# Kernel tuning notes

Measured on AMD Instinct MI355X. Metric: run time of the kernel, lower is better.

The kernel has to match this reference:

```python
import jax, jax.numpy as jnp
import numpy as np

D_IN = 1024
D_OUT = 1024
NUM_HEADS = 16
HEAD_DIM = D_OUT // NUM_HEADS


def setup_inputs() -> dict:
    key = jax.random.key(0)
    ks = jax.random.split(key, 6)
    s = 0.02
    x = jax.random.normal(ks[0], (2, 2048, D_IN), dtype=jnp.float32)
    wq = jax.random.normal(ks[1], (D_IN, D_OUT), dtype=jnp.float32) * s
    wk = jax.random.normal(ks[2], (D_IN, D_OUT), dtype=jnp.float32) * s
    wv = jax.random.normal(ks[3], (D_IN, D_OUT), dtype=jnp.float32) * s
    wo = jax.random.normal(ks[4], (D_OUT, D_OUT), dtype=jnp.float32) * s
    bo = jax.random.normal(ks[5], (D_OUT,), dtype=jnp.float32) * s
    return {"x": x, "wq": wq, "wk": wk, "wv": wv, "wo": wo, "bo": bo}


def reference(x, wq, wk, wv, wo, bo):
    B, S, _ = x.shape
    # QKV projections (no bias, qkv_bias=False)
    def split_heads(t):
        return t.reshape(B, S, NUM_HEADS, HEAD_DIM).transpose(0, 2, 1, 3)  # [B,H,S,Dh]
    q = split_heads(x @ wq)
    k = split_heads(x @ wk)
    v = split_heads(x @ wv)
    scores = jnp.einsum('bhqd,bhkd->bhqk', q, k) / np.sqrt(HEAD_DIM).astype(np.float32)
    causal = jnp.tril(jnp.ones((S, S), dtype=bool))  # [S,S]
    scores = jnp.where(causal[None, None], scores, -jnp.inf)
    attn = jax.nn.softmax(scores, axis=-1)  # dropout p=0.0 -> identity
    ctx = jnp.einsum('bhqk,bhkd->bhqd', attn, v)
    ctx = ctx.transpose(0, 2, 1, 3).reshape(B, S, D_OUT)
    return ctx @ wo + bo
```

## Files before the change

kernel.cpp:

```cpp
#include <hip/hip_runtime.h>

typedef short s16x8 __attribute__((ext_vector_type(8)));
typedef float f32x4 __attribute__((ext_vector_type(4)));
typedef float f32x16 __attribute__((ext_vector_type(16)));
typedef unsigned int u32;
typedef u32 u32x2 __attribute__((ext_vector_type(2)));
typedef u32 u32x4 __attribute__((ext_vector_type(4)));
typedef unsigned short u16;

#define MFMA16(a, b, c) __builtin_amdgcn_mfma_f32_16x16x32_bf16((a), (b), (c), 0, 0, 0)
#define MFMA32(a, b, c) __builtin_amdgcn_mfma_f32_32x32x16_bf16((a), (b), (c), 0, 0, 0)

__device__ __forceinline__ u16 f2bf(float f) {
  unsigned u = __builtin_bit_cast(unsigned, f);
  unsigned r = (u + 0x7FFFu + ((u >> 16) & 1u)) >> 16;
  return (u16)r;
}

__device__ __forceinline__ u32 pack2bf(float lo, float hi) {
  return (u32)f2bf(lo) | ((u32)f2bf(hi) << 16);
}

__device__ __forceinline__ u32 cvtpk(float lo, float hi) {
  u32 r;
  asm("v_cvt_pk_bf16_f32 %0, %1, %2" : "=v"(r) : "v"(lo), "v"(hi));
  return r;
}

__device__ __forceinline__ float bf2f(u32 lo16) {
  return __builtin_bit_cast(float, lo16 << 16);
}

__device__ __forceinline__ void gl_lds16(const u16* g, u16* s) {
  __builtin_amdgcn_global_load_lds(
      (const __attribute__((address_space(1))) void*)g,
      (__attribute__((address_space(3))) void*)s, 16, 0, 0);
}

__global__ __launch_bounds__(256) void cvt_bf16(const float* __restrict__ in,
                                                u16* __restrict__ out, int n4) {
  int i = blockIdx.x * 256 + threadIdx.x;
  if (i < n4) {
    float4 v = reinterpret_cast<const float4*>(in)[i];
    ushort4 o;
    o.x = f2bf(v.x); o.y = f2bf(v.y); o.z = f2bf(v.z); o.w = f2bf(v.w);
    reinterpret_cast<ushort4*>(out)[i] = o;
  }
}

__global__ __launch_bounds__(256) void transp4(const float* __restrict__ wq,
                                               const float* __restrict__ wk,
                                               const float* __restrict__ wv,
                                               const float* __restrict__ wo,
                                               u16* __restrict__ wqkvt,
                                               u16* __restrict__ wot, float qscale) {
  __shared__ float tile[64][65];
  int z = blockIdx.z;
  const float* W = (z == 0) ? wq : (z == 1) ? wk : (z == 2) ? wv : wo;
  u16* out = (z < 3) ? (wqkvt + z * 1048576) : wot;
  float sc = (z == 0) ? qscale : 1.0f;
  int n0 = blockIdx.x * 64, k0 = blockIdx.y * 64;
  int t = threadIdx.x;
#pragma unroll
  for (int i = 0; i < 16; i++) {
    int idx = t + i * 256;
    int r = idx >> 6, c = idx & 63;
    tile[r][c] = W[(k0 + r) * 1024 + (n0 + c)];
  }
  __syncthreads();
#pragma unroll
  for (int i = 0; i < 16; i++) {
    int idx = t + i * 256;
    int r = idx >> 6, c = idx & 63;
    out[(n0 + r) * 1024 + (k0 + c)] = f2bf(tile[c][r] * sc);
  }
}

template <int MODE>
__global__ __launch_bounds__(256, 6) void gemm2(const u16* __restrict__ A,
                                                const u16* __restrict__ Bt,
                                                const float* __restrict__ bias,
                                                void* __restrict__ outp) {
  constexpr int K = 1024, NT = K / 32;
  __shared__ __align__(16) u16 shm[12288];
  int t = threadIdx.x, w = t >> 6, l = t & 63;
  int m0 = blockIdx.y * 64, n0 = blockIdx.x * 128;
  int wm = (w >> 1) * 32, wn = (w & 1) * 64;
  int g = l >> 4, ql = l & 15;
  int xs = (g ^ ((ql >> 1) & 3)) * 8;

  f32x4 acc[2][4];
#pragma unroll
  for (int i = 0; i < 2; i++)
#pragma unroll
    for (int j = 0; j < 4; j++) acc[i][j] = f32x4{0.f, 0.f, 0.f, 0.f};

  int lrow = l >> 2, lcol = ((l & 3) ^ ((l >> 3) & 3)) * 8;
  const u16* Ag0 = A + (m0 + 16 * w + lrow) * K + lcol;
  const u16* Bg0 = Bt + (n0 + 32 * w + lrow) * K + lcol;
  u16* Asw[2] = {shm + 16 * w * 32, shm + 2048 + 16 * w * 32};
  u16* Bsw[2] = {shm + 4096 + 32 * w * 32, shm + 8192 + 32 * w * 32};

#define STAGE(buf, kt)                              \
  do {                                              \
    int k0_ = (kt) * 32;                            \
    gl_lds16(Ag0 + k0_, Asw[buf]);                  \
    gl_lds16(Bg0 + k0_, Bsw[buf]);                  \
    gl_lds16(Bg0 + 16 * K + k0_, Bsw[buf] + 512);   \
  } while (0)

#define COMPUTE(buf)                                                              \
  do {                                                                            \
    const u16* As_ = shm + (buf)*2048;                                            \
    const u16* Bs_ = shm + 4096 + (buf)*4096;                                     \
    s16x8 af[2], bv[4];                                                           \
    _Pragma("unroll") for (int fm = 0; fm < 2; fm++)                              \
        af[fm] = *reinterpret_cast<const s16x8*>(                                 \
            &As_[(wm + fm * 16 + ql) * 32 + xs]);                                 \
    _Pragma("unroll") for (int fn = 0; fn < 4; fn++)                              \
        bv[fn] = *reinterpret_cast<const s16x8*>(                                 \
            &Bs_[(wn + fn * 16 + ql) * 32 + xs]);                                 \
    _Pragma("unroll") for (int fm = 0; fm < 2; fm++)                              \
        _Pragma("unroll") for (int fn = 0; fn < 4; fn++)                          \
            acc[fm][fn] = MFMA16(af[fm], bv[fn], acc[fm][fn]);                    \
  } while (0)

  STAGE(0, 0);
  __syncthreads();
  int cur = 0;
  for (int kt = 0; kt < NT - 1; kt++) {
    STAGE(cur ^ 1, kt + 1);
    COMPUTE(cur);
    __syncthreads();
    cur ^= 1;
  }
  COMPUTE(cur);
#undef STAGE
#undef COMPUTE

  if (MODE == 1) {
#pragma unroll
    for (int fm = 0; fm < 2; fm++)
#pragma unroll
      for (int fn = 0; fn < 4; fn++)
#pragma unroll
        for (int j = 0; j < 4; j++) {
          int m = m0 + wm + fm * 16 + g * 4 + j;
          int n = n0 + wn + fn * 16 + ql;
          ((float*)outp)[m * 1024 + n] = acc[fm][fn][j] + bias[n];
        }
    return;
  }

  __syncthreads();
  u16* tlw = shm + w * 2048;
  int nb = n0 + wn;
  int proj = nb >> 10;
  int nn6 = (nb & 1023) >> 6;

  if (proj < 2) {
    u16* o = (u16*)outp + proj * 4194304;
#pragma unroll
    for (int fm = 0; fm < 2; fm++) {
#pragma unroll
      for (int fn = 0; fn < 4; fn++)
#pragma unroll
        for (int j = 0; j < 4; j++)
          tlw[(g * 4 + j) * 68 + fn * 16 + ql] = f2bf(acc[fm][fn][j]);
#pragma unroll
      for (int i = 0; i < 4; i++) {
        int row = i * 4 + g;
        u32x2 v = *reinterpret_cast<const u32x2*>(tlw + row * 68 + ql * 4);
        int m = m0 + wm + fm * 16 + row;
        int bh = (m >> 11) * 16 + nn6;
        *reinterpret_cast<u32x2*>(o + (bh * 2048 + (m & 2047)) * 64 + ql * 4) = v;
      }
    }
  } else {
    u16* o = (u16*)outp + 8388608;
    int kq = (l & 3) * 4;
    int pr = ((kq & 4) << 1) | ((kq & 8) >> 1);
#pragma unroll
    for (int fm = 0; fm < 2; fm++) {
#pragma unroll
      for (int fn = 0; fn < 4; fn++)
#pragma unroll
        for (int j = 0; j < 4; j++)
          tlw[(g * 4 + j) * 68 + fn * 16 + ql] = f2bf(acc[fm][fn][j]);
      int m = m0 + wm + fm * 16;
      int batch = m >> 11, key0 = m & 2047;
      int bh = batch * 16 + nn6;
#pragma unroll
      for (int i = 0; i < 4; i++) {
        int hd = i * 16 + (l >> 2);
        u16 v0 = tlw[(pr + 0) * 68 + hd];
        u16 v1 = tlw[(pr + 1) * 68 + hd];
        u16 v2 = tlw[(pr + 2) * 68 + hd];
        u16 v3 = tlw[(pr + 3) * 68 + hd];
        u32x2 v;
        v[0] = (u32)v0 | ((u32)v1 << 16);
        v[1] = (u32)v2 | ((u32)v3 << 16);
        *reinterpret_cast<u32x2*>(o + (bh * 64 + hd) * 2048 + key0 + kq) = v;
      }
    }
  }
}

__global__ __launch_bounds__(512, 4) void attn_kernel(const u16* __restrict__ Q,
                                                      const u16* __restrict__ Kb,
                                                      const u16* __restrict__ Vt,
                                                      u16* __restrict__ Ctx,
                                                      u16* __restrict__ part_o,
                                                      float* __restrict__ part_l) {
  __shared__ __align__(16) u16 Kl[2][2048];
  __shared__ __align__(16) u16 Vl[2][2048];
  __shared__ __align__(16) u16 tl[8][32 * 68];
  int tid = threadIdx.x, w = tid >> 6, l = tid & 63;
  int lq = l & 31, h = l >> 5;

  int B = blockIdx.x;
  int head = (B & 7) + 8 * ((B >> 3) & 3);
  int u = B >> 5;
  const signed char QCv[16] = {3, 2, 4, 4, 6, 6, 6, 7, 7, 7, 7, 5, 5, 5, 1, 0};
  const signed char CKv[16] = {0, 0, 0, 1, 0, 1, 2, 0, 1, 2, 3, 0, 1, 2, 0, 0};
  int qc = QCv[u], ck = CKv[u];
  int t0, t1;
  if (qc == 4)      { t0 = ck * 20; t1 = t0 + 20; }
  else if (qc == 5) { t0 = ck * 16; t1 = t0 + 16; }
  else if (qc == 6) { t0 = (ck == 0) ? 0 : (ck == 1) ? 19 : 38;
                      t1 = (ck == 0) ? 19 : (ck == 1) ? 38 : 56; }
  else if (qc == 7) { t0 = ck * 16; t1 = t0 + 16; }
  else              { t0 = 0; t1 = (qc + 1) * 8; }
  int dtile = qc * 8 + w;
  int q0w = qc * 256 + w * 32;
  int q = q0w + lq;

  const u16* Qp = Q + (head * 2048 + q0w) * 64;
  const u16* Kp = Kb + head * 2048 * 64;
  const u16* Vp = Vt + head * 64 * 2048;

  s16x8 qf[4];
#pragma unroll
  for (int f = 0; f < 4; f++)
    qf[f] = *reinterpret_cast<const s16x8*>(Qp + lq * 64 + f * 16 + h * 8);

  const u16* gstage;
  int gstep, ldsoff;
  if (w < 4) {
    int row = w * 8 + (l >> 3);
    int c = (l & 7) ^ (row & 7);
    gstage = Kp + row * 64 + c * 8;
    gstep = 32 * 64;
    ldsoff = w * 512;
  } else {
    int lin = (w - 4) * 64 + l;
    int rp = lin >> 3, pos = lin & 7;
    int d = rp * 2 + (pos >> 2);
    int c = (pos & 3) ^ (rp & 3);
    gstage = Vp + d * 2048 + c * 8;
    gstep = 32;
    ldsoff = (w - 4) * 512;
  }

  f32x16 oacc[2];
#pragma unroll
  for (int dt = 0; dt < 2; dt++)
#pragma unroll
    for (int rr = 0; rr < 16; rr++) oacc[dt][rr] = 0.f;
  float lsum = 0.f;

#define STAGEKV(buf, kt)                                                  \
  gl_lds16(gstage + (kt) * gstep, ((w < 4) ? Kl[buf] : Vl[buf]) + ldsoff)

  STAGEKV(0, t0);
  __syncthreads();
  int cur = 0;

  for (int kt = t0; kt < t1; kt++) {
    if (kt + 1 < t1) STAGEKV(cur ^ 1, kt + 1);

    if (kt <= dtile) {
      s16x8 kc[4];
#pragma unroll
      for (int f = 0; f < 4; f++)
        kc[f] = *reinterpret_cast<const s16x8*>(
            &Kl[cur][lq * 64 + (((f * 2 + h) ^ (lq & 7)) * 8)]);

      f32x16 s;
#pragma unroll
      for (int rr = 0; rr < 16; rr++) s[rr] = 0.f;
      __builtin_amdgcn_s_setprio(1);
#pragma unroll
      for (int f = 0; f < 4; f++) s = MFMA32(kc[f], qf[f], s);
      __builtin_amdgcn_s_setprio(0);

      float p[16];
      if (kt == dtile) {
        int kb = kt * 32;
#pragma unroll
        for (int rr = 0; rr < 16; rr++) {
          int key = kb + (rr & 3) + 8 * (rr >> 2) + 4 * h;
          float e = exp2f(s[rr]);
          p[rr] = (key <= q) ? e : 0.f;
        }
      } else {
#pragma unroll
        for (int rr = 0; rr < 16; rr++) p[rr] = exp2f(s[rr]);
      }
#pragma unroll
      for (int rr = 0; rr < 16; rr++) lsum += p[rr];

      u32 pw[2][4];
#pragma unroll
      for (int kh = 0; kh < 2; kh++)
#pragma unroll
        for (int uu = 0; uu < 4; uu++)
          pw[kh][uu] = cvtpk(p[kh * 8 + 2 * uu], p[kh * 8 + 2 * uu + 1]);

      s16x8 vf[2][2];
#pragma unroll
      for (int dt = 0; dt < 2; dt++)
#pragma unroll
        for (int kh = 0; kh < 2; kh++) {
          int rp = dt * 16 + (lq >> 1);
          int soff = rp * 64 + (lq & 1) * 32 + (((kh * 2 + h) ^ (rp & 3)) * 8);
          vf[dt][kh] = *reinterpret_cast<const s16x8*>(&Vl[cur][soff]);
        }

      __builtin_amdgcn_s_setprio(1);
#pragma unroll
      for (int kh = 0; kh < 2; kh++) {
        s16x8 pf = __builtin_bit_cast(
            s16x8, u32x4{pw[kh][0], pw[kh][1], pw[kh][2], pw[kh][3]});
        oacc[0] = MFMA32(vf[0][kh], pf, oacc[0]);
        oacc[1] = MFMA32(vf[1][kh], pf, oacc[1]);
      }
      __builtin_amdgcn_s_setprio(0);
    }

    __syncthreads();
    cur ^= 1;
  }
#undef STAGEKV

  if (qc >= 4) {
    int base = (qc == 4) ? 0 : (qc == 5) ? 2 : (qc == 6) ? 5 : 8;
    int rec = head * 12 + base + ck;
    u32* po = reinterpret_cast<u32*>(part_o) + (size_t)rec * 8192 + w * 1024 + l * 16;
#pragma unroll
    for (int dt = 0; dt < 2; dt++)
#pragma unroll
      for (int i = 0; i < 8; i++)
        po[dt * 8 + i] = pack2bf(oacc[dt][2 * i], oacc[dt][2 * i + 1]);
    part_l[(size_t)rec * 512 + w * 64 + l] = lsum;
    return;
  }

  float ltot = lsum + __shfl_xor(lsum, 32);
  float invl = 1.0f / ltot;
  u16* myl = tl[w];
#pragma unroll
  for (int dt = 0; dt < 2; dt++)
#pragma unroll
    for (int i = 0; i < 8; i++) {
      int d = ((2 * i) & 3) + 8 * (i >> 1) + 4 * h + dt * 32;
      u32 pkv = pack2bf(oacc[dt][2 * i] * invl, oacc[dt][2 * i + 1] * invl);
      *reinterpret_cast<u32*>(myl + lq * 68 + d) = pkv;
    }

  int b = head >> 4, hh = head & 15;
  int gbase = b * 2048 + q0w;
#pragma unroll
  for (int i = 0; i < 8; i++) {
    int chunkk = i * 64 + l;
    int row = chunkk >> 4, col4 = (chunkk & 15) * 4;
    u32x2 v = *reinterpret_cast<const u32x2*>(myl + row * 68 + col4);
    *reinterpret_cast<u32x2*>(Ctx + (gbase + row) * 1024 + hh * 64 + col4) = v;
  }
}

__global__ __launch_bounds__(256) void attn_combine(const u16* __restrict__ part_o,
                                                    const float* __restrict__ part_l,
                                                    u16* __restrict__ Ctx) {
  __shared__ __align__(16) u16 tl[4][32 * 68];
  int wv = threadIdx.x >> 6, l = threadIdx.x & 63;
  int lq = l & 31, h = l >> 5;
  int unit = blockIdx.x * 4 + wv;
  int head = unit & 31, rest = unit >> 5;
  int qc = 4 + (rest >> 3), w = rest & 7;
  int nc = (qc == 4) ? 2 : (qc == 7) ? 4 : 3;
  int base = (qc == 4) ? 0 : (qc == 5) ? 2 : (qc == 6) ? 5 : 8;
  int rec0 = head * 12 + base;

  float lsum = 0.f;
  float of[32];
#pragma unroll
  for (int i = 0; i < 32; i++) of[i] = 0.f;
  for (int cc = 0; cc < nc; cc++) {
    int rec = rec0 + cc;
    lsum += part_l[(size_t)rec * 512 + w * 64 + l];
    const u32* po =
        reinterpret_cast<const u32*>(part_o) + (size_t)rec * 8192 + w * 1024 + l * 16;
#pragma unroll
    for (int uu = 0; uu < 16; uu++) {
      u32 a = po[uu];
      of[2 * uu] += bf2f(a & 0xFFFFu);
      of[2 * uu + 1] += bf2f(a >> 16);
    }
  }

  float ltot = lsum + __shfl_xor(lsum, 32);
  float invl = 1.0f / ltot;

  u16* myl = tl[wv];
#pragma unroll
  for (int dt = 0; dt < 2; dt++)
#pragma unroll
    for (int i = 0; i < 8; i++) {
      int uu = dt * 8 + i;
      int d = ((2 * i) & 3) + 8 * (i >> 1) + 4 * h + dt * 32;
      *reinterpret_cast<u32*>(myl + lq * 68 + d) =
          pack2bf(of[2 * uu] * invl, of[2 * uu + 1] * invl);
    }

  int b_ = head >> 4, hh = head & 15;
  int gbase = b_ * 2048 + qc * 256 + w * 32;
#pragma unroll
  for (int i = 0; i < 8; i++) {
    int chunkk = i * 64 + l;
    int row = chunkk >> 4, col4 = (chunkk & 15) * 4;
    u32x2 v = *reinterpret_cast<const u32x2*>(myl + row * 68 + col4);
    *reinterpret_cast<u32x2*>(Ctx + (gbase + row) * 1024 + hh * 64 + col4) = v;
  }
}

extern "C" void kernel_launch(void* const* d_in, const int* in_sizes, int n_in,
                              void* d_out, int out_size, void* d_ws, size_t ws_size,
                              hipStream_t stream) {
  const float* x = (const float*)d_in[0];
  const float* wq = (const float*)d_in[1];
  const float* wk = (const float*)d_in[2];
  const float* wv = (const float*)d_in[3];
  const float* wo = (const float*)d_in[4];
  const float* bo = (const float*)d_in[5];

  char* ws = (char*)d_ws;
  const size_t MB = 1 << 20;
  u16* xb    = (u16*)(ws + 0 * MB);
  u16* wqkvt = (u16*)(ws + 8 * MB);
  u16* wot   = (u16*)(ws + 14 * MB);
  u16* qkv   = (u16*)(ws + 16 * MB);
  u16* ctx   = (u16*)(ws + 40 * MB);
  u16* part_o   = (u16*)(ws + 0 * MB);
  float* part_l = (float*)(ws + 12582912);

  const float QSCALE = 0.125f * 1.44269504f;

  cvt_bf16<<<4096, 256, 0, stream>>>(x, xb, 1048576);
  transp4<<<dim3(16, 16, 4), 256, 0, stream>>>(wq, wk, wv, wo, wqkvt, wot, QSCALE);

  gemm2<0><<<dim3(24, 64), 256, 0, stream>>>(xb, wqkvt, nullptr, qkv);

  attn_kernel<<<512, 512, 0, stream>>>(qkv, qkv + 4194304, qkv + 8388608, ctx,
                                       part_o, part_l);
  attn_combine<<<256, 256, 0, stream>>>(part_o, part_l, ctx);

  gemm2<1><<<dim3(8, 64), 256, 0, stream>>>(ctx, wot, bo, d_out);
}
```

Measured before the change: 117.6 us.

## Stage K/V in four-tile windows and merge prep kernels into one launch

The attention kernel now loads four 32-key K/V tiles per stage into a unified 64KB shared buffer and processes them between barriers. This cuts barrier count per key tile by four, in exchange for more LDS per block, which may lower occupancy. The ctx-writeback scratch reuses the same buffer. Separately, the bf16 conversion of x and the weight transposes are fused into one launch to save a kernel launch.

```diff
diff --git a/kernel.cpp b/kernel.cpp
--- a/kernel.cpp
+++ b/kernel.cpp
@@ -37,30 +37,29 @@
       (__attribute__((address_space(3))) void*)s, 16, 0, 0);
 }
 
-__global__ __launch_bounds__(256) void cvt_bf16(const float* __restrict__ in,
-                                                u16* __restrict__ out, int n4) {
-  int i = blockIdx.x * 256 + threadIdx.x;
-  if (i < n4) {
-    float4 v = reinterpret_cast<const float4*>(in)[i];
+__global__ __launch_bounds__(256) void prep(const float* __restrict__ x,
+                                            u16* __restrict__ xb,
+                                            const float* __restrict__ wq,
+                                            const float* __restrict__ wk,
+                                            const float* __restrict__ wv,
+                                            const float* __restrict__ wo,
+                                            u16* __restrict__ wqkvt,
+                                            u16* __restrict__ wot, float qscale) {
+  __shared__ float tile[64][65];
+  int B = blockIdx.x, t = threadIdx.x;
+  if (B < 4096) {
+    int i = B * 256 + t;
+    float4 v = reinterpret_cast<const float4*>(x)[i];
     ushort4 o;
     o.x = f2bf(v.x); o.y = f2bf(v.y); o.z = f2bf(v.z); o.w = f2bf(v.w);
-    reinterpret_cast<ushort4*>(out)[i] = o;
-  }
-}
-
-__global__ __launch_bounds__(256) void transp4(const float* __restrict__ wq,
-                                               const float* __restrict__ wk,
-                                               const float* __restrict__ wv,
-                                               const float* __restrict__ wo,
-                                               u16* __restrict__ wqkvt,
-                                               u16* __restrict__ wot, float qscale) {
-  __shared__ float tile[64][65];
-  int z = blockIdx.z;
-  const float* W = (z == 0) ? wq : (z == 1) ? wk : (z == 2) ? wv : wo;
-  u16* out = (z < 3) ? (wqkvt + z * 1048576) : wot;
-  float sc = (z == 0) ? qscale : 1.0f;
-  int n0 = blockIdx.x * 64, k0 = blockIdx.y * 64;
-  int t = threadIdx.x;
+    reinterpret_cast<ushort4*>(xb)[i] = o;
+    return;
+  }
+  int zz = (B - 4096) >> 8, bb = (B - 4096) & 255;
+  const float* W = (zz == 0) ? wq : (zz == 1) ? wk : (zz == 2) ? wv : wo;
+  u16* out = (zz < 3) ? (wqkvt + zz * 1048576) : wot;
+  float sc = (zz == 0) ? qscale : 1.0f;
+  int n0 = (bb & 15) * 64, k0 = (bb >> 4) * 64;
 #pragma unroll
   for (int i = 0; i < 16; i++) {
     int idx = t + i * 256;
@@ -212,9 +211,7 @@
                                                       u16* __restrict__ Ctx,
                                                       u16* __restrict__ part_o,
                                                       float* __restrict__ part_l) {
-  __shared__ __align__(16) u16 Kl[2][2048];
-  __shared__ __align__(16) u16 Vl[2][2048];
-  __shared__ __align__(16) u16 tl[8][32 * 68];
+  __shared__ __align__(16) u16 shm[32768];
   int tid = threadIdx.x, w = tid >> 6, l = tid & 63;
   int lq = l & 31, h = l >> 5;
 
@@ -222,15 +219,10 @@
   int head = (B & 7) + 8 * ((B >> 3) & 3);
   int u = B >> 5;
   const signed char QCv[16] = {3, 2, 4, 4, 6, 6, 6, 7, 7, 7, 7, 5, 5, 5, 1, 0};
+  const signed char T0W[16] = {0, 0, 0, 5, 0, 5, 10, 0, 4, 8, 12, 0, 4, 8, 0, 0};
+  const signed char NWv[16] = {8, 6, 5, 5, 5, 5, 4, 4, 4, 4, 4, 4, 4, 4, 4, 2};
   const signed char CKv[16] = {0, 0, 0, 1, 0, 1, 2, 0, 1, 2, 3, 0, 1, 2, 0, 0};
-  int qc = QCv[u], ck = CKv[u];
-  int t0, t1;
-  if (qc == 4)      { t0 = ck * 20; t1 = t0 + 20; }
-  else if (qc == 5) { t0 = ck * 16; t1 = t0 + 16; }
-  else if (qc == 6) { t0 = (ck == 0) ? 0 : (ck == 1) ? 19 : 38;
-                      t1 = (ck == 0) ? 19 : (ck == 1) ? 38 : 56; }
-  else if (qc == 7) { t0 = ck * 16; t1 = t0 + 16; }
-  else              { t0 = 0; t1 = (qc + 1) * 8; }
+  int qc = QCv[u], ck = CKv[u], t0w = T0W[u], nw = NWv[u];
   int dtile = qc * 8 + w;
   int q0w = qc * 256 + w * 32;
   int q = q0w + lq;
@@ -259,7 +251,7 @@
     int c = (pos & 3) ^ (rp & 3);
     gstage = Vp + d * 2048 + c * 8;
     gstep = 32;
-    ldsoff = (w - 4) * 512;
+    ldsoff = 8192 + (w - 4) * 512;
   }
 
   f32x16 oacc[2];
@@ -269,79 +261,91 @@
     for (int rr = 0; rr < 16; rr++) oacc[dt][rr] = 0.f;
   float lsum = 0.f;
 
-#define STAGEKV(buf, kt)                                                  \
-  gl_lds16(gstage + (kt) * gstep, ((w < 4) ? Kl[buf] : Vl[buf]) + ldsoff)
-
-  STAGEKV(0, t0);
+#define STAGEW(buf, aw)                                                      \
+  do {                                                                       \
+    u16* sb_ = shm + (buf)*16384 + ldsoff;                                   \
+    _Pragma("unroll") for (int j_ = 0; j_ < 4; j_++)                         \
+        gl_lds16(gstage + ((aw)*4 + j_) * gstep, sb_ + j_ * 2048);           \
+  } while (0)
+
+  STAGEW(0, t0w);
   __syncthreads();
   int cur = 0;
 
-  for (int kt = t0; kt < t1; kt++) {
-    if (kt + 1 < t1) STAGEKV(cur ^ 1, kt + 1);
-
-    if (kt <= dtile) {
-      s16x8 kc[4];
-#pragma unroll
-      for (int f = 0; f < 4; f++)
-        kc[f] = *reinterpret_cast<const s16x8*>(
-            &Kl[cur][lq * 64 + (((f * 2 + h) ^ (lq & 7)) * 8)]);
-
-      f32x16 s;
-#pragma unroll
-      for (int rr = 0; rr < 16; rr++) s[rr] = 0.f;
-      __builtin_amdgcn_s_setprio(1);
-#pragma unroll
-      for (int f = 0; f < 4; f++) s = MFMA32(kc[f], qf[f], s);
-      __builtin_amdgcn_s_setprio(0);
-
-      float p[16];
-      if (kt == dtile) {
-        int kb = kt * 32;
-#pragma unroll
-        for (int rr = 0; rr < 16; rr++) {
-          int key = kb + (rr & 3) + 8 * (rr >> 2) + 4 * h;
-          float e = exp2f(s[rr]);
-          p[rr] = (key <= q) ? e : 0.f;
+  for (int wi = 0; wi < nw; wi++) {
+    if (wi + 1 < nw) STAGEW(cur ^ 1, t0w + wi + 1);
+
+    const u16* kwin = shm + cur * 16384;
+    const u16* vwin = kwin + 8192;
+#pragma unroll
+    for (int j = 0; j < 4; j++) {
+      int kt = (t0w + wi) * 4 + j;
+      if (kt <= dtile) {
+        const u16* ktile = kwin + j * 2048;
+        s16x8 kc[4];
+#pragma unroll
+        for (int f = 0; f < 4; f++)
+          kc[f] = *reinterpret_cast<const s16x8*>(
+              &ktile[lq * 64 + (((f * 2 + h) ^ (lq & 7)) * 8)]);
+
+        f32x16 s;
+#pragma unroll
+        for (int rr = 0; rr < 16; rr++) s[rr] = 0.f;
+        __builtin_amdgcn_s_setprio(1);
+#pragma unroll
+        for (int f = 0; f < 4; f++) s = MFMA32(kc[f], qf[f], s);
+        __builtin_amdgcn_s_setprio(0);
+
+        float p[16];
+        if (kt == dtile) {
+          int kb = kt * 32;
+#pragma unroll
+          for (int rr = 0; rr < 16; rr++) {
+            int key = kb + (rr & 3) + 8 * (rr >> 2) + 4 * h;
+            float e = exp2f(s[rr]);
+            p[rr] = (key <= q) ? e : 0.f;
+          }
+        } else {
+#pragma unroll
+          for (int rr = 0; rr < 16; rr++) p[rr] = exp2f(s[rr]);
         }
-      } else {
-#pragma unroll
-        for (int rr = 0; rr < 16; rr++) p[rr] = exp2f(s[rr]);
+#pragma unroll
+        for (int rr = 0; rr < 16; rr++) lsum += p[rr];
+
+        u32 pw[2][4];
+#pragma unroll
+        for (int kh = 0; kh < 2; kh++)
+#pragma unroll
+          for (int uu = 0; uu < 4; uu++)
+            pw[kh][uu] = cvtpk(p[kh * 8 + 2 * uu], p[kh * 8 + 2 * uu + 1]);
+
+        const u16* vtile = vwin + j * 2048;
+        s16x8 vf[2][2];
+#pragma unroll
+        for (int dt = 0; dt < 2; dt++)
+#pragma unroll
+          for (int kh = 0; kh < 2; kh++) {
+            int rp = dt * 16 + (lq >> 1);
+            int soff = rp * 64 + (lq & 1) * 32 + (((kh * 2 + h) ^ (rp & 3)) * 8);
+            vf[dt][kh] = *reinterpret_cast<const s16x8*>(&vtile[soff]);
+          }
+
+        __builtin_amdgcn_s_setprio(1);
+#pragma unroll
+        for (int kh = 0; kh < 2; kh++) {
+          s16x8 pf = __builtin_bit_cast(
+              s16x8, u32x4{pw[kh][0], pw[kh][1], pw[kh][2], pw[kh][3]});
+          oacc[0] = MFMA32(vf[0][kh], pf, oacc[0]);
+          oacc[1] = MFMA32(vf[1][kh], pf, oacc[1]);
+        }
+        __builtin_amdgcn_s_setprio(0);
       }
-#pragma unroll
-      for (int rr = 0; rr < 16; rr++) lsum += p[rr];
-
-      u32 pw[2][4];
-#pragma unroll
-      for (int kh = 0; kh < 2; kh++)
-#pragma unroll
-        for (int uu = 0; uu < 4; uu++)
-          pw[kh][uu] = cvtpk(p[kh * 8 + 2 * uu], p[kh * 8 + 2 * uu + 1]);
-
-      s16x8 vf[2][2];
-#pragma unroll
-      for (int dt = 0; dt < 2; dt++)
-#pragma unroll
-        for (int kh = 0; kh < 2; kh++) {
-          int rp = dt * 16 + (lq >> 1);
-          int soff = rp * 64 + (lq & 1) * 32 + (((kh * 2 + h) ^ (rp & 3)) * 8);
-          vf[dt][kh] = *reinterpret_cast<const s16x8*>(&Vl[cur][soff]);
-        }
-
-      __builtin_amdgcn_s_setprio(1);
-#pragma unroll
-      for (int kh = 0; kh < 2; kh++) {
-        s16x8 pf = __builtin_bit_cast(
-            s16x8, u32x4{pw[kh][0], pw[kh][1], pw[kh][2], pw[kh][3]});
-        oacc[0] = MFMA32(vf[0][kh], pf, oacc[0]);
-        oacc[1] = MFMA32(vf[1][kh], pf, oacc[1]);
-      }
-      __builtin_amdgcn_s_setprio(0);
     }
 
     __syncthreads();
     cur ^= 1;
   }
-#undef STAGEKV
+#undef STAGEW
 
   if (qc >= 4) {
     int base = (qc == 4) ? 0 : (qc == 5) ? 2 : (qc == 6) ? 5 : 8;
@@ -358,7 +362,7 @@
 
   float ltot = lsum + __shfl_xor(lsum, 32);
   float invl = 1.0f / ltot;
-  u16* myl = tl[w];
+  u16* myl = shm + w * 2176;
 #pragma unroll
   for (int dt = 0; dt < 2; dt++)
 #pragma unroll
@@ -456,8 +460,7 @@
 
   const float QSCALE = 0.125f * 1.44269504f;
 
-  cvt_bf16<<<4096, 256, 0, stream>>>(x, xb, 1048576);
-  transp4<<<dim3(16, 16, 4), 256, 0, stream>>>(wq, wk, wv, wo, wqkvt, wot, QSCALE);
+  prep<<<5120, 256, 0, stream>>>(x, xb, wq, wk, wv, wo, wqkvt, wot, QSCALE);
 
   gemm2<0><<<dim3(24, 64), 256, 0, stream>>>(xb, wqkvt, nullptr, qkv);
 
```

Result: faster. 115.0 us (-2.2%).
